# Kernel tuning notes

Hardware: AMD Instinct MI355X
Metric: run time of the kernel (lower is better)

## Reference

```python
import jax, jax.numpy as jnp
import numpy as np

B, T, H = 8, 2048, 1024

def setup_inputs() -> dict:
    key = jax.random.key(0)
    ks = jax.random.split(key, 7)
    s = 1.0 / np.sqrt(H)
    return {
        "x": jax.random.normal(ks[0], (B, T, H), dtype=jnp.float32),
        "Wq": jax.random.uniform(ks[1], (H, H), jnp.float32, -s, s),
        "bq": jax.random.uniform(ks[2], (H,), jnp.float32, -s, s),
        "Wk": jax.random.uniform(ks[3], (H, H), jnp.float32, -s, s),
        "bk": jax.random.uniform(ks[4], (H,), jnp.float32, -s, s),
        "Wv": jax.random.uniform(ks[5], (H, H), jnp.float32, -s, s),
        "bv": jax.random.uniform(ks[6], (H,), jnp.float32, -s, s),
    }

def reference(x, Wq, bq, Wk, bk, Wv, bv):
    # Linear layers: y = x @ W^T + b (torch convention: store W as [out,in]; here square so use [in,out] directly)
    Q = x @ Wq + bq                      # [B, T, H]
    K = x @ Wk + bk
    V = x @ Wv + bv
    scores = jnp.einsum('bqd,bkd->bqk', Q, K) / jnp.sqrt(jnp.float32(x.shape[-1]))
    # NOTE: original uses nn.Softmax(dim=1) -> softmax over the QUERY axis (axis=1)
    attention = jax.nn.softmax(scores, axis=1)  # [B, T, T]
    out = jnp.einsum('bqk,bkd->bqd', attention, V)
    return out
```

## Files before the change

### kernel.cpp

```cpp
#include <hip/hip_runtime.h>
#include <hip/hip_bf16.h>

typedef __attribute__((ext_vector_type(8))) short short8;
typedef __attribute__((ext_vector_type(4))) float f32x4;

__device__ __forceinline__ float bf2f(unsigned short u) {
    unsigned v = ((unsigned)u) << 16;
    float f;
    __builtin_memcpy(&f, &v, 4);
    return f;
}
__device__ __forceinline__ unsigned short f2bf(float f) {
    unsigned v;
    __builtin_memcpy(&v, &f, 4);
    unsigned r = (v + 0x7fffu + ((v >> 16) & 1u)) >> 16;
    return (unsigned short)r;
}

#define GLD16(g, l)                                                            \
    __builtin_amdgcn_global_load_lds(                                          \
        (const __attribute__((address_space(1))) void*)(g),                    \
        (__attribute__((address_space(3))) void*)(l), 16, 0, 0)

__global__ __launch_bounds__(256) void cast_f32_bf16(const float* __restrict__ in,
                                                     unsigned short* __restrict__ out,
                                                     size_t n) {
    size_t stride = (size_t)gridDim.x * blockDim.x * 4;
    for (size_t i = ((size_t)blockIdx.x * blockDim.x + threadIdx.x) * 4; i < n; i += stride) {
        float4 v = *(const float4*)(in + i);
        ushort4 o;
        o.x = f2bf(v.x); o.y = f2bf(v.y); o.z = f2bf(v.z); o.w = f2bf(v.w);
        *(ushort4*)(out + i) = o;
    }
}

__global__ __launch_bounds__(256) void cast_transpose_w(const float* __restrict__ W,
                                                        unsigned short* __restrict__ WT, int D) {
    __shared__ float tile[32][33];
    int bx = blockIdx.x * 32;
    int by = blockIdx.y * 32;
    int tx = threadIdx.x & 31, ty = threadIdx.x >> 5;
    for (int i = 0; i < 32; i += 8)
        tile[ty + i][tx] = W[(size_t)(by + ty + i) * D + bx + tx];
    __syncthreads();
    for (int i = 0; i < 32; i += 8)
        WT[(size_t)(bx + ty + i) * D + by + tx] = f2bf(tile[tx][ty + i]);
}

__global__ __launch_bounds__(256) void concat3(const float* __restrict__ a,
                                               const float* __restrict__ b,
                                               const float* __restrict__ c,
                                               float* __restrict__ o, int n) {
    int i = blockIdx.x * 256 + threadIdx.x;
    if (i < n) { o[i] = a[i]; o[n + i] = b[i]; o[2 * n + i] = c[i]; }
}

template <int EPI>
__global__ __launch_bounds__(512, 2) void gemm256(
    const unsigned short* __restrict__ A, const unsigned short* __restrict__ B,
    void* __restrict__ Cv, const float* __restrict__ bias,
    int K, float scale, int lda, int ldb, int ldc,
    long sA, long sB, long sC) {
    __shared__ __attribute__((aligned(16))) unsigned short sm[2][2][2][8192];

    const int tid = threadIdx.x;
    const int wv = tid >> 6, lane = tid & 63;
    const int wm = wv >> 2, wn = wv & 3;
    const int r16 = lane & 15, cHi = lane >> 4;
    const int tileM = blockIdx.y * 256, tileN = blockIdx.x * 256;
    const int bz = blockIdx.z;
    A += (size_t)bz * sA;
    B += (size_t)bz * sB;

    size_t offA[2], offB[2];
    int ldsOff[2];
    const int swzsrc = ((lane & 3) ^ ((lane >> 3) & 3)) * 8;
#pragma unroll
    for (int j = 0; j < 2; ++j) {
        int row = (wv * 2 + j) * 16 + (lane >> 2);
        offA[j] = (size_t)(tileM + row) * lda + swzsrc;
        offB[j] = (size_t)(tileN + row) * ldb + swzsrc;
        ldsOff[j] = (wv * 2 + j) * 1024;
    }

#define STAGE_OP(OP, S, KT)                                                     \
    do {                                                                        \
        const unsigned short* _s = (OP) ? B : A;                                \
        const size_t* _o = (OP) ? offB : offA;                                  \
        char* _d = (char*)&sm[((S) >> 1) & 1][(S) & 1][OP][0];                  \
        GLD16(_s + _o[0] + (KT), _d + ldsOff[0]);                               \
        GLD16(_s + _o[1] + (KT), _d + ldsOff[1]);                               \
    } while (0)

    f32x4 acc[8][4];
#pragma unroll
    for (int m = 0; m < 8; ++m)
#pragma unroll
        for (int n = 0; n < 4; ++n) acc[m][n] = (f32x4){0.f, 0.f, 0.f, 0.f};

    const int slotXor = (lane >> 1) & 3;
    const int aBase = (wm * 128 + r16) * 32 + (cHi ^ slotXor) * 8;
    const int bBase = (wn * 64 + r16) * 32 + (cHi ^ slotXor) * 8;

    STAGE_OP(0, 0, 0); STAGE_OP(1, 0, 0);
    STAGE_OP(0, 1, 32); STAGE_OP(1, 1, 32);
    STAGE_OP(0, 2, 64); STAGE_OP(1, 2, 64);
    asm volatile("s_waitcnt vmcnt(8)" ::: "memory");
    __builtin_amdgcn_s_barrier();

    const int nslot = K >> 5;
    for (int H = 0; H < nslot; ++H) {
        const unsigned short* Abuf = &sm[(H >> 1) & 1][H & 1][0][0];
        const unsigned short* Bbuf = &sm[(H >> 1) & 1][H & 1][1][0];

        short8 aF[8], bF[4];
#pragma unroll
        for (int m = 0; m < 8; ++m) aF[m] = *(const short8*)&Abuf[aBase + m * 512];
#pragma unroll
        for (int n = 0; n < 4; ++n) bF[n] = *(const short8*)&Bbuf[bBase + n * 512];

        const int S = H + 3;
        const int kt = ((S << 5) < K) ? (S << 5) : 0;
        STAGE_OP(0, S, kt);
        STAGE_OP(1, S, kt);

        asm volatile("s_waitcnt lgkmcnt(0)" ::: "memory");
        __builtin_amdgcn_sched_barrier(0);
        __builtin_amdgcn_s_setprio(1);
#pragma unroll
        for (int m = 0; m < 8; ++m) {
#pragma unroll
            for (int n = 0; n < 4; ++n)
                acc[m][n] = __builtin_amdgcn_mfma_f32_16x16x32_bf16(aF[m], bF[n], acc[m][n], 0, 0, 0);
        }
        __builtin_amdgcn_s_setprio(0);
        asm volatile("s_waitcnt vmcnt(8)" ::: "memory");
        __builtin_amdgcn_s_barrier();
    }
    asm volatile("s_waitcnt vmcnt(0)" ::: "memory");
#undef STAGE_OP

    const int rowB = tileM + wm * 128 + cHi * 4;
    const int colB = tileN + wn * 64 + r16;
#pragma unroll
    for (int m = 0; m < 8; ++m) {
#pragma unroll
        for (int n = 0; n < 4; ++n) {
            const int col = colB + n * 16;
            float badd = (EPI == 0) ? bias[col] : 0.f;
#pragma unroll
            for (int r = 0; r < 4; ++r) {
                int row = rowB + m * 16 + r;
                float v = acc[m][n][r];
                if (EPI == 0) v += badd;
                if (EPI == 1) v = __expf(v * scale);
                size_t idx = (size_t)bz * sC + (size_t)row * ldc + col;
                if (EPI == 2) ((float*)Cv)[idx] = v;
                else ((unsigned short*)Cv)[idx] = f2bf(v);
            }
        }
    }
}

__global__ __launch_bounds__(256) void col_sum_partial(const unsigned short* __restrict__ E,
                                                       float* __restrict__ partial, int T) {
    int b = blockIdx.z;
    int k = blockIdx.x * 256 + threadIdx.x;
    int q0 = blockIdx.y * 64;
    const unsigned short* p = E + (size_t)b * T * T + (size_t)q0 * T + k;
    float sum = 0.f;
#pragma unroll 4
    for (int q = 0; q < 64; ++q)
        sum += bf2f(p[(size_t)q * T]);
    partial[((size_t)b * gridDim.y + blockIdx.y) * T + k] = sum;
}

__global__ __launch_bounds__(256) void col_sum_reduce(const float* __restrict__ partial,
                                                      float* __restrict__ invl, int T, int nchunk) {
    int b = blockIdx.y;
    int k = blockIdx.x * 256 + threadIdx.x;
    float s = 0.f;
    for (int c = 0; c < nchunk; ++c)
        s += partial[((size_t)b * nchunk + c) * T + k];
    invl[(size_t)b * T + k] = 1.0f / s;
}

__global__ __launch_bounds__(256) void transpose_scale_bf16(
    const unsigned short* __restrict__ V, const float* __restrict__ invl,
    unsigned short* __restrict__ Vt, int T, int H, int ldv) {
    __shared__ unsigned short tile[64][66];
    int b = blockIdx.z;
    const unsigned short* Vb = V + (size_t)b * T * ldv;
    unsigned short* Vtb = Vt + (size_t)b * H * T;
    const float* il = invl + (size_t)b * T;
    int x0 = blockIdx.x * 64;
    int y0 = blockIdx.y * 64;
    int t = threadIdx.x;
    for (int i = 0; i < 16; ++i) {
        int idx = t + i * 256;
        int r = idx >> 6, c = idx & 63;
        tile[r][c] = Vb[(size_t)(y0 + r) * ldv + x0 + c];
    }
    __syncthreads();
    for (int i = 0; i < 16; ++i) {
        int idx = t + i * 256;
        int r = idx >> 6, c = idx & 63;
        float v = bf2f(tile[c][r]) * il[y0 + c];
        Vtb[(size_t)(x0 + r) * T + y0 + c] = f2bf(v);
    }
}

extern "C" void kernel_launch(void* const* d_in, const int* in_sizes, int n_in,
                              void* d_out, int out_size, void* d_ws, size_t ws_size,
                              hipStream_t stream) {
    const int B = 8, T = 2048, H = 1024;
    const size_t MT = (size_t)B * T;
    const int H3 = 3 * H;

    const float* x  = (const float*)d_in[0];
    const float* Wq = (const float*)d_in[1];
    const float* bq = (const float*)d_in[2];
    const float* Wk = (const float*)d_in[3];
    const float* bk = (const float*)d_in[4];
    const float* Wv = (const float*)d_in[5];
    const float* bv = (const float*)d_in[6];
    float* out = (float*)d_out;

    char* ws = (char*)d_ws;
    size_t o = 0;
    unsigned short* xb   = (unsigned short*)(ws + o); o += MT * H * 2;
    unsigned short* Wcat = (unsigned short*)(ws + o); o += (size_t)H3 * H * 2;
    float* bcat          = (float*)(ws + o);          o += (size_t)H3 * 4;
    unsigned short* QKVb = (unsigned short*)(ws + o); o += MT * H3 * 2;
    unsigned short* Eb   = (unsigned short*)(ws + o); o += (size_t)B * T * T * 2;
    float* partial       = (float*)(ws + o);          o += (size_t)B * 32 * T * 4;
    float* invl          = (float*)(ws + o);          o += (size_t)B * T * 4;
    unsigned short* Vt   = xb;

    cast_f32_bf16<<<2048, 256, 0, stream>>>(x, xb, MT * H);
    dim3 wgrid(32, 32);
    cast_transpose_w<<<wgrid, 256, 0, stream>>>(Wq, Wcat, H);
    cast_transpose_w<<<wgrid, 256, 0, stream>>>(Wk, Wcat + (size_t)H * H, H);
    cast_transpose_w<<<wgrid, 256, 0, stream>>>(Wv, Wcat + (size_t)2 * H * H, H);
    concat3<<<4, 256, 0, stream>>>(bq, bk, bv, bcat, H);

    gemm256<0><<<dim3(H3 / 256, MT / 256, 1), 512, 0, stream>>>(
        xb, Wcat, QKVb, bcat, H, 1.f, H, H, H3, 0, 0, 0);

    gemm256<1><<<dim3(T / 256, T / 256, B), 512, 0, stream>>>(
        QKVb, QKVb + H, Eb, nullptr, H, 0.03125f, H3, H3, T,
        (long)T * H3, (long)T * H3, (long)T * T);

    col_sum_partial<<<dim3(T / 256, 32, B), 256, 0, stream>>>(Eb, partial, T);
    col_sum_reduce<<<dim3(T / 256, B), 256, 0, stream>>>(partial, invl, T, 32);

    transpose_scale_bf16<<<dim3(H / 64, T / 64, B), 256, 0, stream>>>(
        QKVb + 2 * H, invl, Vt, T, H, H3);

    gemm256<2><<<dim3(H / 256, T / 256, B), 512, 0, stream>>>(
        Eb, Vt, out, nullptr, T, 1.f, T, T, H,
        (long)T * T, (long)H * T, (long)T * H);

    (void)in_sizes; (void)n_in; (void)out_size; (void)ws_size;
}
```

Before: 326.9 us.

## Replace 4-stage LDS prefetch ring with double buffer and split B-fragment loads

Shrinks the shared-memory ring from four stages to two (sm[2][2][8192]), so each iteration prefetches only the next k-slice and waits for all outstanding global loads before the barrier. B fragments are now loaded in two halves, with the second pair read while the first MFMA batch runs, which cuts live fragment registers. The intent is lower LDS and register pressure for better occupancy and scheduling. The cost is a shallower prefetch that hides less global-load latency, since vmcnt(0) now stalls every iteration.

```diff
diff --git a/kernel.cpp b/kernel.cpp
--- a/kernel.cpp
+++ b/kernel.cpp
@@ -61,7 +61,7 @@
     void* __restrict__ Cv, const float* __restrict__ bias,
     int K, float scale, int lda, int ldb, int ldc,
     long sA, long sB, long sC) {
-    __shared__ __attribute__((aligned(16))) unsigned short sm[2][2][2][8192];
+    __shared__ __attribute__((aligned(16))) unsigned short sm[2][2][8192];
 
     const int tid = threadIdx.x;
     const int wv = tid >> 6, lane = tid & 63;
@@ -83,13 +83,14 @@
         ldsOff[j] = (wv * 2 + j) * 1024;
     }
 
-#define STAGE_OP(OP, S, KT)                                                     \
+#define STAGE(BUF, KT)                                                          \
     do {                                                                        \
-        const unsigned short* _s = (OP) ? B : A;                                \
-        const size_t* _o = (OP) ? offB : offA;                                  \
-        char* _d = (char*)&sm[((S) >> 1) & 1][(S) & 1][OP][0];                  \
-        GLD16(_s + _o[0] + (KT), _d + ldsOff[0]);                               \
-        GLD16(_s + _o[1] + (KT), _d + ldsOff[1]);                               \
+        char* _dA = (char*)&sm[BUF][0][0];                                      \
+        char* _dB = (char*)&sm[BUF][1][0];                                      \
+        GLD16(A + offA[0] + (KT), _dA + ldsOff[0]);                             \
+        GLD16(A + offA[1] + (KT), _dA + ldsOff[1]);                             \
+        GLD16(B + offB[0] + (KT), _dB + ldsOff[0]);                             \
+        GLD16(B + offB[1] + (KT), _dB + ldsOff[1]);                             \
     } while (0)
 
     f32x4 acc[8][4];
@@ -102,43 +103,49 @@
     const int aBase = (wm * 128 + r16) * 32 + (cHi ^ slotXor) * 8;
     const int bBase = (wn * 64 + r16) * 32 + (cHi ^ slotXor) * 8;
 
-    STAGE_OP(0, 0, 0); STAGE_OP(1, 0, 0);
-    STAGE_OP(0, 1, 32); STAGE_OP(1, 1, 32);
-    STAGE_OP(0, 2, 64); STAGE_OP(1, 2, 64);
-    asm volatile("s_waitcnt vmcnt(8)" ::: "memory");
+    STAGE(0, 0);
+    asm volatile("s_waitcnt vmcnt(0)" ::: "memory");
     __builtin_amdgcn_s_barrier();
 
-    const int nslot = K >> 5;
-    for (int H = 0; H < nslot; ++H) {
-        const unsigned short* Abuf = &sm[(H >> 1) & 1][H & 1][0][0];
-        const unsigned short* Bbuf = &sm[(H >> 1) & 1][H & 1][1][0];
-
-        short8 aF[8], bF[4];
+    short8 aF[8], bF0, bF1;
+    const int nt = K >> 5;
+    for (int t = 0; t < nt; ++t) {
+        const int cur = t & 1, nxt = cur ^ 1;
+        const int ktn = (t + 1 == nt) ? 0 : ((t + 1) << 5);
+        const unsigned short* Abuf = &sm[cur][0][0];
+        const unsigned short* Bbuf = &sm[cur][1][0];
+
 #pragma unroll
         for (int m = 0; m < 8; ++m) aF[m] = *(const short8*)&Abuf[aBase + m * 512];
-#pragma unroll
-        for (int n = 0; n < 4; ++n) bF[n] = *(const short8*)&Bbuf[bBase + n * 512];
-
-        const int S = H + 3;
-        const int kt = ((S << 5) < K) ? (S << 5) : 0;
-        STAGE_OP(0, S, kt);
-        STAGE_OP(1, S, kt);
-
+        bF0 = *(const short8*)&Bbuf[bBase];
+        bF1 = *(const short8*)&Bbuf[bBase + 512];
+        STAGE(nxt, ktn);
         asm volatile("s_waitcnt lgkmcnt(0)" ::: "memory");
         __builtin_amdgcn_sched_barrier(0);
         __builtin_amdgcn_s_setprio(1);
 #pragma unroll
         for (int m = 0; m < 8; ++m) {
-#pragma unroll
-            for (int n = 0; n < 4; ++n)
-                acc[m][n] = __builtin_amdgcn_mfma_f32_16x16x32_bf16(aF[m], bF[n], acc[m][n], 0, 0, 0);
+            acc[m][0] = __builtin_amdgcn_mfma_f32_16x16x32_bf16(aF[m], bF0, acc[m][0], 0, 0, 0);
+            acc[m][1] = __builtin_amdgcn_mfma_f32_16x16x32_bf16(aF[m], bF1, acc[m][1], 0, 0, 0);
         }
         __builtin_amdgcn_s_setprio(0);
-        asm volatile("s_waitcnt vmcnt(8)" ::: "memory");
+
+        bF0 = *(const short8*)&Bbuf[bBase + 1024];
+        bF1 = *(const short8*)&Bbuf[bBase + 1536];
+        asm volatile("s_waitcnt lgkmcnt(0)" ::: "memory");
+        __builtin_amdgcn_sched_barrier(0);
+        __builtin_amdgcn_s_setprio(1);
+#pragma unroll
+        for (int m = 0; m < 8; ++m) {
+            acc[m][2] = __builtin_amdgcn_mfma_f32_16x16x32_bf16(aF[m], bF0, acc[m][2], 0, 0, 0);
+            acc[m][3] = __builtin_amdgcn_mfma_f32_16x16x32_bf16(aF[m], bF1, acc[m][3], 0, 0, 0);
+        }
+        __builtin_amdgcn_s_setprio(0);
+
+        asm volatile("s_waitcnt vmcnt(0)" ::: "memory");
         __builtin_amdgcn_s_barrier();
     }
-    asm volatile("s_waitcnt vmcnt(0)" ::: "memory");
-#undef STAGE_OP
+#undef STAGE
 
     const int rowB = tileM + wm * 128 + cHi * 4;
     const int colB = tileN + wn * 64 + r16;
```

New measurement: 335.0 us. 1.02x slower.
